# Kernel tuning notes

Hardware: AMD Instinct MI355X
Metric: run time of the kernel (lower is better)

The kernel has to match this reference:

```python
import jax, jax.numpy as jnp
import numpy as np

B, N, K = 8, 8192, 8192   # batch, out_features, in_features
PACK = 8
# maybe_pack_idxs places original column offset POS[b] into nibble b
POS = [0, 2, 4, 6, 1, 3, 5, 7]
# inverse permutation: original offset p comes from nibble INV[p]
INV = jnp.array([0, 4, 1, 5, 2, 6, 3, 7], dtype=jnp.int32)


def setup_inputs() -> dict:
    key = jax.random.key(0)
    k1, k2 = jax.random.split(key)
    x = jax.random.normal(k1, (B, K), dtype=jnp.float32)
    # random 4-bit codebook indices, then pack exactly like maybe_pack_idxs
    idxs = jax.random.randint(k2, (N, K), 0, 16, dtype=jnp.int32)
    g = idxs.reshape(N, K // PACK, PACK)
    packed = jnp.zeros((N, K // PACK), dtype=jnp.int32)
    for b, p in enumerate(POS):
        packed = packed + (g[..., p] << jnp.int32(4 * b))
    return {"input": x, "Qidxs": packed}


def decompress_weight(Qidxs):
    # Qidxs: [N, K/8] int32 -> W: [N, K] float32
    shifts = (jnp.arange(PACK, dtype=jnp.int32) * 4)
    nibbles = (Qidxs[..., None] >> shifts) & 0xF       # [N, K/8, 8], nibble order
    unpacked = nibbles[..., INV]                        # restore original column order
    # grid = arange(-8, 8) + 0.5  =>  value = idx - 7.5
    return unpacked.reshape(N, K).astype(jnp.float32) - 7.5


def reference(input, Qidxs):
    W = decompress_weight(Qidxs)          # [N, K]
    return input @ W.T                    # [B, N]
```

## Files before the change

### kernel.cpp

```cpp
#include <hip/hip_runtime.h>
#include <hip/hip_fp16.h>
#include <stdint.h>


typedef _Float16 half8 __attribute__((ext_vector_type(8)));
typedef float floatx16 __attribute__((ext_vector_type(16)));

union H2U { unsigned u; __half2 h; };
union V4H8 { uint4 u4; half8 h8; };

__device__ __forceinline__ unsigned unpack_even(unsigned ws, __half2 c1, __half2 c2) {
    H2U t; t.u = (ws & 0x000F000Fu) | 0x64006400u;
    t.h = __hadd2(__hadd2(t.h, c1), c2);
    return t.u;
}
__device__ __forceinline__ unsigned unpack_odd(unsigned ws, __half2 cs, __half2 cc) {
    H2U t; t.u = (ws & 0x00F000F0u) | 0x64006400u;
    t.h = __hfma2(t.h, cs, cc);
    return t.u;
}

#define BPITCH 136
#define BBUF   (32 * BPITCH)
#define APITCH 272
#define ATBL   (16 * APITCH)
#define WLDS   (BBUF + ATBL)
#define NW     16
#define LDS_BYTES (NW * WLDS)

__global__ __launch_bounds__(1024, 4)
void hi4b_gemm(const float* __restrict__ x, const int* __restrict__ q,
               float* __restrict__ out)
{
    extern __shared__ char lds[];
    const int tid  = threadIdx.x;
    const int lane = tid & 63;
    const int wv   = tid >> 6;
    const int n0   = blockIdx.x * 32;

    const int nlo = lane & 31;
    const int u   = lane >> 5;
    const int sh  = 8 * u;
    const int c   = lane & 7;
    const int r0  = lane >> 3;

    const uint4*  q4 = (const uint4*)q;
    const float4* x4 = (const float4*)x;

    const int qbase = (n0 + r0) * 256 + wv * 16 + c;
    const int slot = lane & 15, shi = lane >> 4;
    const int uu = slot >> 3, rr = slot & 7;
    const int xbase = rr * 2048 + wv * 128 + uu;

    char* Bw = lds + wv * WLDS;
    char* Aw = Bw + BBUF;

    if (lane < 16)
        *(uint4*)(Aw + lane * APITCH + 256) = make_uint4(0u, 0u, 0u, 0u);

    uint4 rb0, rb1, rb2, rb3;
    float4 ra[8];

    auto loadB = [&](int sc) {
        int b = qbase + sc * 8;
        rb0 = q4[b];
        rb1 = q4[b +  8 * 256];
        rb2 = q4[b + 16 * 256];
        rb3 = q4[b + 24 * 256];
    };
    auto writeB = [&]() {
        char* p0 = Bw + (r0     ) * BPITCH + c * 16;
        char* p1 = Bw + (r0 +  8) * BPITCH + c * 16;
        char* p2 = Bw + (r0 + 16) * BPITCH + c * 16;
        char* p3 = Bw + (r0 + 24) * BPITCH + c * 16;
        *(uint2*)(p0)     = make_uint2(rb0.x, rb0.y);
        *(uint2*)(p0 + 8) = make_uint2(rb0.z, rb0.w);
        *(uint2*)(p1)     = make_uint2(rb1.x, rb1.y);
        *(uint2*)(p1 + 8) = make_uint2(rb1.z, rb1.w);
        *(uint2*)(p2)     = make_uint2(rb2.x, rb2.y);
        *(uint2*)(p2 + 8) = make_uint2(rb2.z, rb2.w);
        *(uint2*)(p3)     = make_uint2(rb3.x, rb3.y);
        *(uint2*)(p3 + 8) = make_uint2(rb3.z, rb3.w);
    };
    auto loadA = [&](int sc) {
        #pragma unroll
        for (int i = 0; i < 4; ++i) {
            int s = 4 * i + shi;
            int xi = xbase + sc * 64 + 4 * s;
            ra[2 * i]     = x4[xi];
            ra[2 * i + 1] = x4[xi + 2];
        }
    };
    auto writeA = [&]() {
        #pragma unroll
        for (int i = 0; i < 4; ++i) {
            int s = 4 * i + shi;
            H2U a0, a1, a2, a3;
            a0.h = __floats2half2_rn(ra[2*i].x,   ra[2*i].y);
            a1.h = __floats2half2_rn(ra[2*i].z,   ra[2*i].w);
            a2.h = __floats2half2_rn(ra[2*i+1].x, ra[2*i+1].y);
            a3.h = __floats2half2_rn(ra[2*i+1].z, ra[2*i+1].w);
            *(uint4*)(Aw + s * APITCH + slot * 16) = make_uint4(a0.u, a1.u, a2.u, a3.u);
        }
    };

    const __half2 c1 = __floats2half2_rn(-1024.0f, -1024.0f);
    const __half2 c2 = __floats2half2_rn(-7.5f, -7.5f);
    const __half2 cs = __floats2half2_rn(0.0625f, 0.0625f);
    const __half2 cc = __floats2half2_rn(-71.5f, -71.5f);

    floatx16 acc;
    #pragma unroll
    for (int i = 0; i < 16; ++i) acc[i] = 0.0f;

    const int aoff = (nlo < 8) ? (u * 8 + nlo) * 16 : 256;
    const char* ap = Aw + aoff;
    const char* bp = Bw + nlo * BPITCH;

    auto compute = [&]() {
        #pragma unroll
        for (int s = 0; s < 16; ++s) {
            uint2 w2 = *(const uint2*)(bp + s * 8);
            V4H8 A;  A.u4 = *(const uint4*)(ap + s * APITCH);
            unsigned wsa = w2.x >> sh;
            unsigned wsb = w2.y >> sh;
            V4H8 Bf;
            Bf.u4.x = unpack_even(wsa, c1, c2);
            Bf.u4.y = unpack_odd (wsa, cs, cc);
            Bf.u4.z = unpack_even(wsb, c1, c2);
            Bf.u4.w = unpack_odd (wsb, cs, cc);
            acc = __builtin_amdgcn_mfma_f32_32x32x16_f16(A.h8, Bf.h8, acc, 0, 0, 0);
        }
    };

    loadB(0); loadA(0);
    writeB(); writeA();
    loadB(1); loadA(1);
    compute();
    writeB(); writeA();
    compute();

    __syncthreads();
    {
        float* red = (float*)lds + wv * 256;
        #pragma unroll
        for (int r = 0; r < 4; ++r)
            red[(r + 4 * u) * 32 + nlo] = acc[r];
    }
    __syncthreads();
    if (tid < 256) {
        const int b = tid >> 5, nl = tid & 31;
        const float* rd = (const float*)lds;
        float sm = 0.0f;
        #pragma unroll
        for (int w = 0; w < NW; ++w)
            sm += rd[w * 256 + b * 32 + nl];
        out[b * 8192 + n0 + nl] = sm;
    }
}

extern "C" void kernel_launch(void* const* d_in, const int* in_sizes, int n_in,
                              void* d_out, int out_size, void* d_ws, size_t ws_size,
                              hipStream_t stream)
{
    const float* x = (const float*)d_in[0];
    const int*   q = (const int*)d_in[1];
    float* out = (float*)d_out;

    hipLaunchKernelGGL(hi4b_gemm, dim3(256), dim3(1024), LDS_BYTES, stream,
                       x, q, out);
}
```

Baseline: 16.10 us.

## Precompute fp16 activation table in a prepass kernel and load A fragments from global

Adds a small prepass kernel that converts x to fp16 once and writes it to workspace in the MFMA fragment layout, padding included. The GEMM kernel then reads A fragments straight from global/L2 into registers instead of every block redoing the fp32 load, conversion and LDS staging. This removes redundant conversion work and LDS traffic across 256 blocks and shrinks LDS use, but adds a second kernel launch and a dependency between the kernels. It also makes every wave issue 16-byte global loads for A.

```diff
diff --git a/kernel.cpp b/kernel.cpp
--- a/kernel.cpp
+++ b/kernel.cpp
@@ -22,14 +22,30 @@
 
 #define BPITCH 136
 #define BBUF   (32 * BPITCH)
-#define APITCH 272
-#define ATBL   (16 * APITCH)
-#define WLDS   (BBUF + ATBL)
 #define NW     16
-#define LDS_BYTES (NW * WLDS)
+#define LDS_BYTES (NW * BBUF)
+#define TPITCH 272
+
+__global__ void build_atable(const float* __restrict__ x, char* __restrict__ tbl)
+{
+    const int gid  = blockIdx.x * 256 + threadIdx.x;
+    const int S    = gid >> 4, slot = gid & 15;
+    const int uu   = slot >> 3, rr = slot & 7;
+    const float4* x4 = (const float4*)x;
+    float4 fa = x4[rr * 2048 + 4 * S + uu];
+    float4 fb = x4[rr * 2048 + 4 * S + 2 + uu];
+    H2U a0, a1, a2, a3;
+    a0.h = __floats2half2_rn(fa.x, fa.y);
+    a1.h = __floats2half2_rn(fa.z, fa.w);
+    a2.h = __floats2half2_rn(fb.x, fb.y);
+    a3.h = __floats2half2_rn(fb.z, fb.w);
+    *(uint4*)(tbl + S * TPITCH + slot * 16) = make_uint4(a0.u, a1.u, a2.u, a3.u);
+    if (slot == 0)
+        *(uint4*)(tbl + S * TPITCH + 256) = make_uint4(0u, 0u, 0u, 0u);
+}
 
 __global__ __launch_bounds__(1024, 4)
-void hi4b_gemm(const float* __restrict__ x, const int* __restrict__ q,
+void hi4b_gemm(const char* __restrict__ atbl, const int* __restrict__ q,
                float* __restrict__ out)
 {
     extern __shared__ char lds[];
@@ -44,23 +60,15 @@
     const int c   = lane & 7;
     const int r0  = lane >> 3;
 
-    const uint4*  q4 = (const uint4*)q;
-    const float4* x4 = (const float4*)x;
+    const uint4* q4 = (const uint4*)q;
+    const int qbase = (n0 + r0) * 256 + wv * 16 + c;
 
-    const int qbase = (n0 + r0) * 256 + wv * 16 + c;
-    const int slot = lane & 15, shi = lane >> 4;
-    const int uu = slot >> 3, rr = slot & 7;
-    const int xbase = rr * 2048 + wv * 128 + uu;
+    char* Bw = lds + wv * BBUF;
 
-    char* Bw = lds + wv * WLDS;
-    char* Aw = Bw + BBUF;
-
-    if (lane < 16)
-        *(uint4*)(Aw + lane * APITCH + 256) = make_uint4(0u, 0u, 0u, 0u);
+    const int aslot = (nlo < 8) ? (u * 8 + nlo) : 16;
+    const char* ab = atbl + (wv * 32) * TPITCH + aslot * 16;
 
     uint4 rb0, rb1, rb2, rb3;
-    float4 ra[8];
-
     auto loadB = [&](int sc) {
         int b = qbase + sc * 8;
         rb0 = q4[b];
@@ -82,26 +90,13 @@
         *(uint2*)(p3)     = make_uint2(rb3.x, rb3.y);
         *(uint2*)(p3 + 8) = make_uint2(rb3.z, rb3.w);
     };
-    auto loadA = [&](int sc) {
+
+    uint4 TA[8], TB[8];
+    auto loadA = [&](uint4 (&T)[8], int tile) {
+        const char* p = ab + tile * (8 * TPITCH);
         #pragma unroll
-        for (int i = 0; i < 4; ++i) {
-            int s = 4 * i + shi;
-            int xi = xbase + sc * 64 + 4 * s;
-            ra[2 * i]     = x4[xi];
-            ra[2 * i + 1] = x4[xi + 2];
-        }
-    };
-    auto writeA = [&]() {
-        #pragma unroll
-        for (int i = 0; i < 4; ++i) {
-            int s = 4 * i + shi;
-            H2U a0, a1, a2, a3;
-            a0.h = __floats2half2_rn(ra[2*i].x,   ra[2*i].y);
-            a1.h = __floats2half2_rn(ra[2*i].z,   ra[2*i].w);
-            a2.h = __floats2half2_rn(ra[2*i+1].x, ra[2*i+1].y);
-            a3.h = __floats2half2_rn(ra[2*i+1].z, ra[2*i+1].w);
-            *(uint4*)(Aw + s * APITCH + slot * 16) = make_uint4(a0.u, a1.u, a2.u, a3.u);
-        }
+        for (int i = 0; i < 8; ++i)
+            T[i] = *(const uint4*)(p + i * TPITCH);
     };
 
     const __half2 c1 = __floats2half2_rn(-1024.0f, -1024.0f);
@@ -113,15 +108,13 @@
     #pragma unroll
     for (int i = 0; i < 16; ++i) acc[i] = 0.0f;
 
-    const int aoff = (nlo < 8) ? (u * 8 + nlo) * 16 : 256;
-    const char* ap = Aw + aoff;
     const char* bp = Bw + nlo * BPITCH;
 
-    auto compute = [&]() {
+    auto compute8 = [&](uint4 (&T)[8], int s0) {
         #pragma unroll
-        for (int s = 0; s < 16; ++s) {
-            uint2 w2 = *(const uint2*)(bp + s * 8);
-            V4H8 A;  A.u4 = *(const uint4*)(ap + s * APITCH);
+        for (int i = 0; i < 8; ++i) {
+            uint2 w2 = *(const uint2*)(bp + (s0 + i) * 8);
+            V4H8 A;  A.u4 = T[i];
             unsigned wsa = w2.x >> sh;
             unsigned wsb = w2.y >> sh;
             V4H8 Bf;
@@ -133,12 +126,18 @@
         }
     };
 
-    loadB(0); loadA(0);
-    writeB(); writeA();
-    loadB(1); loadA(1);
-    compute();
-    writeB(); writeA();
-    compute();
+    loadB(0);
+    loadA(TA, 0);
+    loadA(TB, 1);
+    writeB();
+    loadB(1);
+    compute8(TA, 0);
+    loadA(TA, 2);
+    compute8(TB, 8);
+    writeB();
+    loadA(TB, 3);
+    compute8(TA, 0);
+    compute8(TB, 8);
 
     __syncthreads();
     {
@@ -166,7 +165,9 @@
     const float* x = (const float*)d_in[0];
     const int*   q = (const int*)d_in[1];
     float* out = (float*)d_out;
+    char*  tbl = (char*)d_ws;
 
+    hipLaunchKernelGGL(build_atable, dim3(32), dim3(256), 0, stream, x, tbl);
     hipLaunchKernelGGL(hi4b_gemm, dim3(256), dim3(1024), LDS_BYTES, stream,
-                       x, q, out);
+                       tbl, q, out);
 }
```

After: 17.63 us. 1.1x slower.
